# Kernel optimization log

Hardware: AMD Instinct MI355X
Metric: run time of the kernel (lower is better)

## Reference

```python
import jax, jax.numpy as jnp
import numpy as np

NUM_HEADS = 16


def setup_inputs() -> dict:
    key = jax.random.key(0)
    ks = jax.random.split(key, 5)
    B, S, E = 4, 2048, 1024
    scale = 1.0 / np.sqrt(E)
    return {
        "x": jax.random.normal(ks[0], (B, S, E), dtype=jnp.float32),
        "w_in": jax.random.normal(ks[1], (E, 3 * E), dtype=jnp.float32) * scale,
        "b_in": jax.random.normal(ks[2], (3 * E,), dtype=jnp.float32) * 0.02,
        "w_out": jax.random.normal(ks[3], (E, E), dtype=jnp.float32) * scale,
        "b_out": jax.random.normal(ks[4], (E,), dtype=jnp.float32) * 0.02,
    }


def reference(x, w_in, b_in, w_out, b_out):
    B, S, E = x.shape
    H = NUM_HEADS
    D = E // H  # head dim
    qkv = x @ w_in + b_in                      # [B,S,3E]
    q, k, v = jnp.split(qkv, 3, axis=-1)       # each [B,S,E]
    q = q.reshape(B, S, H, D)
    k = k.reshape(B, S, H, D)
    v = v.reshape(B, S, H, D)
    # scores scaled by 1/sqrt(D); note: original's causal masked_fill is a
    # no-op (not in-place), so attention is unmasked.
    scores = jnp.einsum("bqhd,bkhd->bhqk", q, k) / jnp.sqrt(jnp.float32(D))
    attn = jax.nn.softmax(scores, axis=-1)      # [B,H,S,S]
    out = jnp.einsum("bhqk,bkhd->bqhd", attn, v).reshape(B, S, E)
    return out @ w_out + b_out
```

## Files before the change

kernel.cpp:

```cpp
#include <hip/hip_runtime.h>
#include <math.h>

#define B_ 4
#define S_ 2048
#define E_ 1024
#define H_ 16
#define D_ 64
#define M_ (B_ * S_)

using f32x4  = __attribute__((ext_vector_type(4))) float;
using short8 = __attribute__((ext_vector_type(8))) short;
using half8  = __attribute__((ext_vector_type(8))) _Float16;
using ushort8_t = __attribute__((ext_vector_type(8))) unsigned short;

__device__ inline unsigned short f2h(float f) {
    _Float16 h = (_Float16)f;
    unsigned short u; __builtin_memcpy(&u, &h, 2); return u;
}
__device__ inline unsigned pk2h(float a, float b) {
    auto t = __builtin_amdgcn_cvt_pkrtz(a, b);
    unsigned u; __builtin_memcpy(&u, &t, 4); return u;
}
__device__ inline float ex2(float x) {
#if __has_builtin(__builtin_amdgcn_exp2f)
    return __builtin_amdgcn_exp2f(x);
#else
    return exp2f(x);
#endif
}
__device__ inline f32x4 mfma16(short8 a, short8 b, f32x4 c) {
    half8 ha, hb;
    __builtin_memcpy(&ha, &a, 16);
    __builtin_memcpy(&hb, &b, 16);
    return __builtin_amdgcn_mfma_f32_16x16x32_f16(ha, hb, c, 0, 0, 0);
}
__device__ inline void gload_lds16(const void* g, void* l) {
    __builtin_amdgcn_global_load_lds(
        (const __attribute__((address_space(1))) void*)g,
        (__attribute__((address_space(3))) void*)l, 16, 0, 0);
}

#define QSCALE 0.18033688f

__global__ __launch_bounds__(256)
void cvt_f16_kernel(const float* __restrict__ X,
                    unsigned short* __restrict__ Xh)
{
    const size_t i = ((size_t)blockIdx.x * 256 + threadIdx.x) * 4;
    float4 v = *(const float4*)(X + i);
    ushort4 h;
    h.x = f2h(v.x);
    h.y = f2h(v.y);
    h.z = f2h(v.z);
    h.w = f2h(v.w);
    *(ushort4*)(Xh + i) = h;
}

__global__ __launch_bounds__(256)
void transpose_cvt_kernel(const float* __restrict__ W,
                          unsigned short* __restrict__ Th, int R, int C)
{
    __shared__ float t[32][33];
    const int tx = threadIdx.x & 31, ty = threadIdx.x >> 5;
    const int c0 = blockIdx.x * 32, r0 = blockIdx.y * 32;
    #pragma unroll
    for (int i = 0; i < 4; ++i)
        t[ty + 8 * i][tx] = W[(size_t)(r0 + ty + 8 * i) * C + c0 + tx];
    __syncthreads();
    #pragma unroll
    for (int i = 0; i < 4; ++i) {
        float v = t[tx][ty + 8 * i];
        Th[(size_t)(c0 + ty + 8 * i) * R + r0 + tx] = f2h(v);
    }
}

template<int OUT_MODE>
__global__ __launch_bounds__(256)
void gemm_mfma_kernel(const unsigned short* __restrict__ Ah,
                      const unsigned short* __restrict__ Bt,
                      const float* __restrict__ bias,
                      float* __restrict__ Cf,
                      unsigned short* __restrict__ Ch,
                      int M, int N, int K)
{
    __shared__ unsigned short As[128][64];
    __shared__ unsigned short Bs[128][64];

    const int tid  = threadIdx.x;
    const int lane = tid & 63;
    const int wave = tid >> 6;
    const int wm = (wave >> 1) * 64, wn = (wave & 1) * 64;
    const int ln = lane & 15, qd = lane >> 4;
    const int m0 = blockIdx.x * 128, n0 = blockIdx.y * 128;

    f32x4 acc[4][4] = {};

    const int srow_l = lane >> 3;
    const int scol   = ((lane & 7) ^ srow_l) * 8;
    const int swz    = (ln & 7) * 8;

    for (int k0 = 0; k0 < K; k0 += 64) {
        #pragma unroll
        for (int c = 0; c < 4; ++c) {
            const int r = wave * 32 + c * 8;
            const size_t ga = (size_t)(m0 + r + srow_l) * K + k0 + scol;
            const size_t gb = (size_t)(n0 + r + srow_l) * K + k0 + scol;
            gload_lds16(Ah + ga, &As[r][0]);
            gload_lds16(Bt + gb, &Bs[r][0]);
        }
        __syncthreads();

        #pragma unroll
        for (int ks = 0; ks < 2; ++ks) {
            const int co = (ks * 32 + qd * 8) ^ swz;
            short8 aa[4], bb[4];
            #pragma unroll
            for (int mt = 0; mt < 4; ++mt)
                aa[mt] = *(const short8*)&As[wm + mt * 16 + ln][co];
            #pragma unroll
            for (int nt = 0; nt < 4; ++nt)
                bb[nt] = *(const short8*)&Bs[wn + nt * 16 + ln][co];
            __builtin_amdgcn_s_setprio(1);
            #pragma unroll
            for (int mt = 0; mt < 4; ++mt)
                #pragma unroll
                for (int nt = 0; nt < 4; ++nt)
                    acc[mt][nt] = mfma16(aa[mt], bb[nt], acc[mt][nt]);
            __builtin_amdgcn_s_setprio(0);
        }
        __syncthreads();
    }

    #pragma unroll
    for (int nt = 0; nt < 4; ++nt) {
        const int col = n0 + wn + nt * 16 + ln;
        const float bv = bias[col];
        const float scale = (OUT_MODE == 2 && col < E_) ? QSCALE : 1.0f;
        #pragma unroll
        for (int mt = 0; mt < 4; ++mt) {
            #pragma unroll
            for (int r = 0; r < 4; ++r) {
                const int row = m0 + wm + mt * 16 + qd * 4 + r;
                float f = acc[mt][nt][r] + bv;
                size_t idx = (size_t)row * N + col;
                if (OUT_MODE == 0) Cf[idx] = f;
                else               Ch[idx] = f2h(f * scale);
            }
        }
    }
}

__global__ __launch_bounds__(256)
void attn_mfma_kernel(const unsigned short* __restrict__ qkvh,
                      unsigned short* __restrict__ outh)
{
    constexpr int TQ = 128, TK = 64, LD = 64;
    __shared__ unsigned short Ksh[TK][LD];
    __shared__ unsigned short VthA[D_][LD];
    __shared__ unsigned short VthB[D_][LD];

    const int tid  = threadIdx.x;
    const int lane = tid & 63;
    const int wave = tid >> 6;
    const int ln = lane & 15, qd = lane >> 4;
    const int id   = blockIdx.x;
    const int g    = id & 63;
    const int qblk = id >> 6;
    const int h    = g & 15;
    const int b    = g >> 4;
    const int wq0 = wave * 32;
    const int swz = (ln & 7) * 8;

    short8 ones8;
    #pragma unroll
    for (int j = 0; j < 8; ++j) ones8[j] = (short)0x3C00;

    short8 qh[2][2];
    #pragma unroll
    for (int qt = 0; qt < 2; ++qt)
        #pragma unroll
        for (int ks = 0; ks < 2; ++ks) {
            size_t base = ((size_t)(b * S_ + qblk * TQ + wq0 + qt * 16 + ln)) * (3 * E_)
                        + h * 64 + ks * 32 + qd * 8;
            qh[qt][ks] = *(const short8*)(qkvh + base);
        }

    f32x4 o[4][2] = {};
    f32x4 ol[2]   = {};
    short8 pBp[2][2] = {};

    const int krow = tid >> 2, kcol = (tid & 3) * 16;
    const int kswz = (krow & 7) * 8;
    const int vkey = (tid & 31) * 2, vdc = (tid >> 5) * 8;
    const int vslot = (vkey & 0x23) | ((vkey & 0x0C) << 1) | ((vkey & 0x10) >> 2);

    {
        ushort8_t z = {};
        unsigned short* p = &VthB[0][0];
        *(ushort8_t*)(p + tid * 8)        = z;
        *(ushort8_t*)(p + 2048 + tid * 8) = z;
    }

    ushort8_t pk0, pk1, pv0, pv1;
    {
        size_t gb = ((size_t)(b * S_ + krow)) * (3 * E_) + E_ + h * 64 + kcol;
        pk0 = *(const ushort8_t*)(qkvh + gb);
        pk1 = *(const ushort8_t*)(qkvh + gb + 8);
        size_t vb0 = ((size_t)(b * S_ + vkey)) * (3 * E_) + 2 * E_ + h * 64 + vdc;
        pv0 = *(const ushort8_t*)(qkvh + vb0);
        pv1 = *(const ushort8_t*)(qkvh + vb0 + 3 * E_);
    }

    #define TILE_BODY(VW, VR, PREFETCH_KB, DO_PREFETCH)                        \
    {                                                                          \
        *(ushort8_t*)&Ksh[krow][kcol ^ kswz]       = pk0;                      \
        *(ushort8_t*)&Ksh[krow][(kcol + 8) ^ kswz] = pk1;                      \
        _Pragma("unroll")                                                      \
        for (int j = 0; j < 8; ++j)                                            \
            *(unsigned*)&VW[vdc + j][vslot ^ (j * 8)] =                        \
                (unsigned)pv0[j] | ((unsigned)pv1[j] << 16);                   \
        __syncthreads();                                                       \
        if (DO_PREFETCH) {                                                     \
            size_t gb_ = ((size_t)(b * S_ + (PREFETCH_KB) + krow)) * (3 * E_)  \
                       + E_ + h * 64 + kcol;                                   \
            pk0 = *(const ushort8_t*)(qkvh + gb_);                             \
            pk1 = *(const ushort8_t*)(qkvh + gb_ + 8);                         \
            size_t vb_ = ((size_t)(b * S_ + (PREFETCH_KB) + vkey)) * (3 * E_)  \
                       + 2 * E_ + h * 64 + vdc;                                \
            pv0 = *(const ushort8_t*)(qkvh + vb_);                             \
            pv1 = *(const ushort8_t*)(qkvh + vb_ + 3 * E_);                    \
        }                                                                      \
        f32x4 st[4][2] = {};                                                   \
        _Pragma("unroll")                                                      \
        for (int ks = 0; ks < 2; ++ks) {                                       \
            const int co = (ks * 32 + qd * 8) ^ swz;                           \
            short8 kh[4];                                                      \
            _Pragma("unroll")                                                  \
            for (int kt = 0; kt < 4; ++kt)                                     \
                kh[kt] = *(const short8*)&Ksh[kt * 16 + ln][co];               \
            __builtin_amdgcn_s_setprio(1);                                     \
            _Pragma("unroll")                                                  \
            for (int kt = 0; kt < 4; ++kt)                                     \
                _Pragma("unroll")                                              \
                for (int qt = 0; qt < 2; ++qt)                                 \
                    st[kt][qt] = mfma16(kh[kt], qh[qt][ks], st[kt][qt]);       \
            __builtin_amdgcn_s_setprio(0);                                     \
        }                                                                      \
                \
        _Pragma("unroll")                                                      \
        for (int ks = 0; ks < 2; ++ks) {                                       \
            const int co = (ks * 32 + qd * 8) ^ swz;                           \
            short8 vA[4];                                                      \
            _Pragma("unroll")                                                  \
            for (int dt = 0; dt < 4; ++dt)                                     \
                vA[dt] = *(const short8*)&VR[dt * 16 + ln][co];                \
            __builtin_amdgcn_s_setprio(1);                                     \
            _Pragma("unroll")                                                  \
            for (int dt = 0; dt < 4; ++dt)                                     \
                _Pragma("unroll")                                              \
                for (int qt = 0; qt < 2; ++qt)                                 \
                    o[dt][qt] = mfma16(vA[dt], pBp[ks][qt], o[dt][qt]);        \
            _Pragma("unroll")                                                  \
            for (int qt = 0; qt < 2; ++qt)                                     \
                ol[qt] = mfma16(ones8, pBp[ks][qt], ol[qt]);                   \
            __builtin_amdgcn_s_setprio(0);                                     \
        }                                                                      \
                             \
        _Pragma("unroll")                                                      \
        for (int qt = 0; qt < 2; ++qt)                                         \
            _Pragma("unroll")                                                  \
            for (int ks = 0; ks < 2; ++ks) {                                   \
                unsigned w_[4];                                                \
                w_[0] = pk2h(ex2(st[2 * ks][qt][0]), ex2(st[2 * ks][qt][1]));  \
                w_[1] = pk2h(ex2(st[2 * ks][qt][2]), ex2(st[2 * ks][qt][3]));  \
                w_[2] = pk2h(ex2(st[2 * ks + 1][qt][0]),                       \
                             ex2(st[2 * ks + 1][qt][1]));                      \
                w_[3] = pk2h(ex2(st[2 * ks + 1][qt][2]),                       \
                             ex2(st[2 * ks + 1][qt][3]));                      \
                __builtin_memcpy(&pBp[ks][qt], w_, 16);                        \
            }                                                                  \
        __syncthreads();                                                       \
    }

    for (int kb = 0; kb < S_; kb += 2 * TK) {
        TILE_BODY(VthA, VthB, kb + TK, true);
        TILE_BODY(VthB, VthA, kb + 2 * TK, (kb + 2 * TK < S_));
    }
    #undef TILE_BODY

    #pragma unroll
    for (int ks = 0; ks < 2; ++ks) {
        const int co = (ks * 32 + qd * 8) ^ swz;
        short8 vA[4];
        #pragma unroll
        for (int dt = 0; dt < 4; ++dt)
            vA[dt] = *(const short8*)&VthB[dt * 16 + ln][co];
        #pragma unroll
        for (int dt = 0; dt < 4; ++dt)
            #pragma unroll
            for (int qt = 0; qt < 2; ++qt)
                o[dt][qt] = mfma16(vA[dt], pBp[ks][qt], o[dt][qt]);
        #pragma unroll
        for (int qt = 0; qt < 2; ++qt)
            ol[qt] = mfma16(ones8, pBp[ks][qt], ol[qt]);
    }

    float inv[2];
    #pragma unroll
    for (int qt = 0; qt < 2; ++qt)
        inv[qt] = 1.0f / ol[qt][0];
    #pragma unroll
    for (int qt = 0; qt < 2; ++qt) {
        const int q = qblk * TQ + wq0 + qt * 16 + ln;
        #pragma unroll
        for (int dt = 0; dt < 4; ++dt) {
            size_t base = ((size_t)(b * S_ + q)) * E_ + h * 64 + dt * 16 + qd * 4;
            ushort4 hh;
            #pragma unroll
            for (int r = 0; r < 4; ++r)
                ((unsigned short*)&hh)[r] = f2h(o[dt][qt][r] * inv[qt]);
            *(ushort4*)(outh + base) = hh;
        }
    }
}

extern "C" void kernel_launch(void* const* d_in, const int* in_sizes, int n_in,
                              void* d_out, int out_size, void* d_ws, size_t ws_size,
                              hipStream_t stream)
{
    const float* x     = (const float*)d_in[0];
    const float* w_in  = (const float*)d_in[1];
    const float* b_in  = (const float*)d_in[2];
    const float* w_out = (const float*)d_in[3];
    const float* b_out = (const float*)d_in[4];
    float* outp = (float*)d_out;

    char* ws = (char*)d_ws;
    unsigned short* qkvh  = (unsigned short*)ws;
    unsigned short* attnh = qkvh  + (size_t)M_ * 3 * E_;
    unsigned short* xh    = attnh + (size_t)M_ * E_;
    unsigned short* wInTh  = attnh;
    unsigned short* wOutTh = qkvh;

    cvt_f16_kernel<<<dim3((M_ * E_) / (4 * 256)), 256, 0, stream>>>(x, xh);

    transpose_cvt_kernel<<<dim3(3 * E_ / 32, E_ / 32), 256, 0, stream>>>(
        w_in, wInTh, E_, 3 * E_);

    gemm_mfma_kernel<2><<<dim3(M_ / 128, (3 * E_) / 128), 256, 0, stream>>>(
        xh, wInTh, b_in, nullptr, qkvh, M_, 3 * E_, E_);

    attn_mfma_kernel<<<dim3((S_ / 128) * H_ * B_), 256, 0, stream>>>(
        qkvh, attnh);

    transpose_cvt_kernel<<<dim3(E_ / 32, E_ / 32), 256, 0, stream>>>(
        w_out, wOutTh, E_, E_);

    gemm_mfma_kernel<0><<<dim3(M_ / 128, E_ / 128), 256, 0, stream>>>(
        attnh, wOutTh, b_out, outp, nullptr, M_, E_, E_);
}
```

Before: 278.7 us.

## Merge prep conversions into one kernel and double attention query tile per block

Folds the input conversion and both weight transpose-conversions into a single launch, and moves w_out's transposed copy to its own workspace slot so it no longer overwrites qkv. The attention kernel now processes 256 queries per block with 512 threads, and the loading of each K/V tile is split so four waves fetch K while the other four fetch V. Each staged K/V tile is therefore reused by twice as many query rows and fewer blocks run. The cost is fewer blocks to spread across CUs (512), higher register and occupancy pressure per CU, and a larger barrier across 8 waves.

New measurement: 267.8 us. 1.04x faster.

```diff
diff --git a/kernel.cpp b/kernel.cpp
--- a/kernel.cpp
+++ b/kernel.cpp
@@ -43,35 +43,39 @@
 #define QSCALE 0.18033688f
 
 __global__ __launch_bounds__(256)
-void cvt_f16_kernel(const float* __restrict__ X,
-                    unsigned short* __restrict__ Xh)
-{
-    const size_t i = ((size_t)blockIdx.x * 256 + threadIdx.x) * 4;
-    float4 v = *(const float4*)(X + i);
-    ushort4 h;
-    h.x = f2h(v.x);
-    h.y = f2h(v.y);
-    h.z = f2h(v.z);
-    h.w = f2h(v.w);
-    *(ushort4*)(Xh + i) = h;
-}
-
-__global__ __launch_bounds__(256)
-void transpose_cvt_kernel(const float* __restrict__ W,
-                          unsigned short* __restrict__ Th, int R, int C)
+void prep_kernel(const float* __restrict__ x,     unsigned short* __restrict__ xh,
+                 const float* __restrict__ w_in,  unsigned short* __restrict__ wInTh,
+                 const float* __restrict__ w_out, unsigned short* __restrict__ wOutTh)
 {
     __shared__ float t[32][33];
-    const int tx = threadIdx.x & 31, ty = threadIdx.x >> 5;
-    const int c0 = blockIdx.x * 32, r0 = blockIdx.y * 32;
+    const int bid  = blockIdx.x;
+    const int tidx = threadIdx.x;
+    if (bid < (M_ * E_) / 1024) {
+        const size_t i = ((size_t)bid * 256 + tidx) * 4;
+        float4 v = *(const float4*)(x + i);
+        ushort4 hh;
+        hh.x = f2h(v.x); hh.y = f2h(v.y); hh.z = f2h(v.z); hh.w = f2h(v.w);
+        *(ushort4*)(xh + i) = hh;
+        return;
+    }
+    const float* W; unsigned short* T; int C, c0, r0;
+    if (bid < 8192 + 3072) {
+        const int t2 = bid - 8192;
+        W = w_in;  T = wInTh;  C = 3 * E_;
+        c0 = (t2 % 96) * 32;  r0 = (t2 / 96) * 32;
+    } else {
+        const int t2 = bid - 11264;
+        W = w_out; T = wOutTh; C = E_;
+        c0 = (t2 & 31) * 32;  r0 = (t2 >> 5) * 32;
+    }
+    const int tx = tidx & 31, ty = tidx >> 5;
     #pragma unroll
     for (int i = 0; i < 4; ++i)
         t[ty + 8 * i][tx] = W[(size_t)(r0 + ty + 8 * i) * C + c0 + tx];
     __syncthreads();
     #pragma unroll
-    for (int i = 0; i < 4; ++i) {
-        float v = t[tx][ty + 8 * i];
-        Th[(size_t)(c0 + ty + 8 * i) * R + r0 + tx] = f2h(v);
-    }
+    for (int i = 0; i < 4; ++i)
+        T[(size_t)(c0 + ty + 8 * i) * E_ + r0 + tx] = f2h(t[tx][ty + 8 * i]);
 }
 
 template<int OUT_MODE>
@@ -150,11 +154,11 @@
     }
 }
 
-__global__ __launch_bounds__(256)
+__global__ __launch_bounds__(512)
 void attn_mfma_kernel(const unsigned short* __restrict__ qkvh,
                       unsigned short* __restrict__ outh)
 {
-    constexpr int TQ = 128, TK = 64, LD = 64;
+    constexpr int TQ = 256, TK = 64, LD = 64;
     __shared__ unsigned short Ksh[TK][LD];
     __shared__ unsigned short VthA[D_][LD];
     __shared__ unsigned short VthB[D_][LD];
@@ -189,23 +193,23 @@
     f32x4 ol[2]   = {};
     short8 pBp[2][2] = {};
 
-    const int krow = tid >> 2, kcol = (tid & 3) * 16;
+    const int stid = tid & 255;
+    const int krow = stid >> 2, kcol = (stid & 3) * 16;
     const int kswz = (krow & 7) * 8;
-    const int vkey = (tid & 31) * 2, vdc = (tid >> 5) * 8;
+    const int vkey = (stid & 31) * 2, vdc = (stid >> 5) * 8;
     const int vslot = (vkey & 0x23) | ((vkey & 0x0C) << 1) | ((vkey & 0x10) >> 2);
 
     {
         ushort8_t z = {};
-        unsigned short* p = &VthB[0][0];
-        *(ushort8_t*)(p + tid * 8)        = z;
-        *(ushort8_t*)(p + 2048 + tid * 8) = z;
-    }
-
-    ushort8_t pk0, pk1, pv0, pv1;
-    {
+        *(ushort8_t*)(&VthB[0][0] + tid * 8) = z;
+    }
+
+    ushort8_t pk0 = {}, pk1 = {}, pv0 = {}, pv1 = {};
+    if (wave < 4) {
         size_t gb = ((size_t)(b * S_ + krow)) * (3 * E_) + E_ + h * 64 + kcol;
         pk0 = *(const ushort8_t*)(qkvh + gb);
         pk1 = *(const ushort8_t*)(qkvh + gb + 8);
+    } else {
         size_t vb0 = ((size_t)(b * S_ + vkey)) * (3 * E_) + 2 * E_ + h * 64 + vdc;
         pv0 = *(const ushort8_t*)(qkvh + vb0);
         pv1 = *(const ushort8_t*)(qkvh + vb0 + 3 * E_);
@@ -213,22 +217,28 @@
 
     #define TILE_BODY(VW, VR, PREFETCH_KB, DO_PREFETCH)                        \
     {                                                                          \
-        *(ushort8_t*)&Ksh[krow][kcol ^ kswz]       = pk0;                      \
-        *(ushort8_t*)&Ksh[krow][(kcol + 8) ^ kswz] = pk1;                      \
-        _Pragma("unroll")                                                      \
-        for (int j = 0; j < 8; ++j)                                            \
-            *(unsigned*)&VW[vdc + j][vslot ^ (j * 8)] =                        \
-                (unsigned)pv0[j] | ((unsigned)pv1[j] << 16);                   \
+        if (wave < 4) {                                                        \
+            *(ushort8_t*)&Ksh[krow][kcol ^ kswz]       = pk0;                  \
+            *(ushort8_t*)&Ksh[krow][(kcol + 8) ^ kswz] = pk1;                  \
+        } else {                                                               \
+            _Pragma("unroll")                                                  \
+            for (int j = 0; j < 8; ++j)                                        \
+                *(unsigned*)&VW[vdc + j][vslot ^ (j * 8)] =                    \
+                    (unsigned)pv0[j] | ((unsigned)pv1[j] << 16);               \
+        }                                                                      \
         __syncthreads();                                                       \
         if (DO_PREFETCH) {                                                     \
-            size_t gb_ = ((size_t)(b * S_ + (PREFETCH_KB) + krow)) * (3 * E_)  \
-                       + E_ + h * 64 + kcol;                                   \
-            pk0 = *(const ushort8_t*)(qkvh + gb_);                             \
-            pk1 = *(const ushort8_t*)(qkvh + gb_ + 8);                         \
-            size_t vb_ = ((size_t)(b * S_ + (PREFETCH_KB) + vkey)) * (3 * E_)  \
-                       + 2 * E_ + h * 64 + vdc;                                \
-            pv0 = *(const ushort8_t*)(qkvh + vb_);                             \
-            pv1 = *(const ushort8_t*)(qkvh + vb_ + 3 * E_);                    \
+            if (wave < 4) {                                                    \
+                size_t gb_ = ((size_t)(b * S_ + (PREFETCH_KB) + krow))         \
+                           * (3 * E_) + E_ + h * 64 + kcol;                    \
+                pk0 = *(const ushort8_t*)(qkvh + gb_);                         \
+                pk1 = *(const ushort8_t*)(qkvh + gb_ + 8);                     \
+            } else {                                                           \
+                size_t vb_ = ((size_t)(b * S_ + (PREFETCH_KB) + vkey))         \
+                           * (3 * E_) + 2 * E_ + h * 64 + vdc;                 \
+                pv0 = *(const ushort8_t*)(qkvh + vb_);                         \
+                pv1 = *(const ushort8_t*)(qkvh + vb_ + 3 * E_);                \
+            }                                                                  \
         }                                                                      \
         f32x4 st[4][2] = {};                                                   \
         _Pragma("unroll")                                                      \
@@ -336,25 +346,20 @@
     float* outp = (float*)d_out;
 
     char* ws = (char*)d_ws;
-    unsigned short* qkvh  = (unsigned short*)ws;
-    unsigned short* attnh = qkvh  + (size_t)M_ * 3 * E_;
-    unsigned short* xh    = attnh + (size_t)M_ * E_;
+    unsigned short* qkvh   = (unsigned short*)ws;
+    unsigned short* attnh  = qkvh   + (size_t)M_ * 3 * E_;
+    unsigned short* xh     = attnh  + (size_t)M_ * E_;
+    unsigned short* wOutTh = xh     + (size_t)M_ * E_;
     unsigned short* wInTh  = attnh;
-    unsigned short* wOutTh = qkvh;
-
-    cvt_f16_kernel<<<dim3((M_ * E_) / (4 * 256)), 256, 0, stream>>>(x, xh);
-
-    transpose_cvt_kernel<<<dim3(3 * E_ / 32, E_ / 32), 256, 0, stream>>>(
-        w_in, wInTh, E_, 3 * E_);
+
+    prep_kernel<<<dim3(8192 + 3072 + 1024), 256, 0, stream>>>(
+        x, xh, w_in, wInTh, w_out, wOutTh);
 
     gemm_mfma_kernel<2><<<dim3(M_ / 128, (3 * E_) / 128), 256, 0, stream>>>(
         xh, wInTh, b_in, nullptr, qkvh, M_, 3 * E_, E_);
 
-    attn_mfma_kernel<<<dim3((S_ / 128) * H_ * B_), 256, 0, stream>>>(
+    attn_mfma_kernel<<<dim3((S_ / 256) * H_ * B_), 512, 0, stream>>>(
         qkvh, attnh);
-
-    transpose_cvt_kernel<<<dim3(E_ / 32, E_ / 32), 256, 0, stream>>>(
-        w_out, wOutTh, E_, E_);
 
     gemm_mfma_kernel<0><<<dim3(M_ / 128, E_ / 128), 256, 0, stream>>>(
         attnh, wOutTh, b_out, outp, nullptr, M_, E_, E_);
```
